# Kernel tuning notes

Measured on AMD Instinct MI355X. Metric: run time of the kernel, lower is better.

Reference implementation:

```python
import jax, jax.numpy as jnp
import numpy as np

EPS_NORM = 1e-12  # torch F.normalize eps
EPS_MM = 1e-08    # min-max denom eps


def setup_inputs() -> dict:
    key = jax.random.key(0)
    k1, k2 = jax.random.split(key)
    global_query = jax.random.normal(k1, (16, 256), dtype=jnp.float32)
    value = jax.random.normal(k2, (16, 256, 128, 128), dtype=jnp.float32)
    return {"global_query": global_query, "value": value}


def reference(global_query, value):
    # L2 normalize (torch.F.normalize: x / max(||x||, eps))
    q = global_query / jnp.maximum(
        jnp.linalg.norm(global_query, axis=-1, keepdims=True), EPS_NORM)
    v = value / jnp.maximum(
        jnp.linalg.norm(value, axis=1, keepdims=True), EPS_NORM)
    B, D, W, H = v.shape
    # score[b, w, h] = sum_d q[b,d] * v[b,d,w,h]  -> [B, W*H]
    score = jnp.einsum('bd,bdwh->bwh', q, v).reshape(B, W * H)
    # min/max computed under no_grad in the original -> stop_gradient
    max_s = jax.lax.stop_gradient(jnp.max(score, axis=1, keepdims=True))
    min_s = jax.lax.stop_gradient(jnp.min(score, axis=1, keepdims=True))
    attn = (score - min_s) / (max_s - min_s + EPS_MM)  # [B, W*H]
    attn = attn.reshape(B, 1, W, H)
    context = attn * v
    return (context, attn)
```

## Files before the change

### kernel.cpp

```cpp
#include <hip/hip_runtime.h>
#include <hip/hip_bf16.h>


#define B_  16
#define D_  256
#define WH_ 16384

__device__ __forceinline__ unsigned int fmap(float f) {
    unsigned int u = __float_as_uint(f);
    return (u & 0x80000000u) ? ~u : (u | 0x80000000u);
}
__device__ __forceinline__ float funmap(unsigned int u) {
    unsigned int b = (u & 0x80000000u) ? (u ^ 0x80000000u) : ~u;
    return __uint_as_float(b);
}

typedef float f32x4_t __attribute__((ext_vector_type(4)));
__device__ __forceinline__ void nt_store4(float* p, float4 v) {
    f32x4_t w = {v.x, v.y, v.z, v.w};
    __builtin_nontemporal_store(w, (f32x4_t*)p);
}

__global__ void init_mm_kernel(unsigned int* __restrict__ mm) {
    int i = threadIdx.x;
    if (i < 2 * B_) mm[i] = (i & 1) ? 0u : 0xFFFFFFFFu;
}

__global__ __launch_bounds__(256) void score_kernel(
    const float* __restrict__ q, const float* __restrict__ value,
    float* __restrict__ score, float* __restrict__ invn,
    unsigned int* __restrict__ mm)
{
    const int b   = blockIdx.y;
    const int tid = threadIdx.x;
    __shared__ float qs[D_];
    __shared__ float red[256];

    float qv = q[b * D_ + tid];
    red[tid] = qv * qv;
    __syncthreads();
    for (int s = 128; s > 0; s >>= 1) {
        if (tid < s) red[tid] += red[tid + s];
        __syncthreads();
    }
    float qnorm2 = red[0];
    __syncthreads();
    qs[tid] = qv * (1.0f / fmaxf(sqrtf(qnorm2), 1e-12f));
    __syncthreads();

    const int wh0 = (blockIdx.x * 256 + tid) * 4;
    const float* vb = value + (size_t)b * D_ * WH_ + wh0;
    float ss0 = 0.f, ss1 = 0.f, ss2 = 0.f, ss3 = 0.f;
    float dt0 = 0.f, dt1 = 0.f, dt2 = 0.f, dt3 = 0.f;
#pragma unroll 4
    for (int d = 0; d < D_; ++d) {
        float4 v4 = *(const float4*)(vb + (size_t)d * WH_);
        float qd = qs[d];
        ss0 += v4.x * v4.x; ss1 += v4.y * v4.y;
        ss2 += v4.z * v4.z; ss3 += v4.w * v4.w;
        dt0 += qd * v4.x;   dt1 += qd * v4.y;
        dt2 += qd * v4.z;   dt3 += qd * v4.w;
    }
    float n0 = 1.0f / fmaxf(sqrtf(ss0), 1e-12f);
    float n1 = 1.0f / fmaxf(sqrtf(ss1), 1e-12f);
    float n2 = 1.0f / fmaxf(sqrtf(ss2), 1e-12f);
    float n3 = 1.0f / fmaxf(sqrtf(ss3), 1e-12f);
    float s0 = dt0 * n0, s1 = dt1 * n1, s2 = dt2 * n2, s3 = dt3 * n3;

    *(float4*)(score + (size_t)b * WH_ + wh0) = make_float4(s0, s1, s2, s3);
    *(float4*)(invn  + (size_t)b * WH_ + wh0) = make_float4(n0, n1, n2, n3);

    float mn = fminf(fminf(s0, s1), fminf(s2, s3));
    float mx = fmaxf(fmaxf(s0, s1), fmaxf(s2, s3));
    red[tid] = mn;
    __syncthreads();
    for (int s = 128; s > 0; s >>= 1) {
        if (tid < s) red[tid] = fminf(red[tid], red[tid + s]);
        __syncthreads();
    }
    float bmn = red[0];
    __syncthreads();
    red[tid] = mx;
    __syncthreads();
    for (int s = 128; s > 0; s >>= 1) {
        if (tid < s) red[tid] = fmaxf(red[tid], red[tid + s]);
        __syncthreads();
    }
    if (tid == 0) {
        atomicMin(&mm[2 * b],     fmap(bmn));
        atomicMax(&mm[2 * b + 1], fmap(red[0]));
    }
}

__global__ __launch_bounds__(256) void ctx_kernel(
    const float* __restrict__ value, const float* __restrict__ score,
    const float* __restrict__ invn, const unsigned int* __restrict__ mm,
    float* __restrict__ out_ctx, float* __restrict__ out_attn)
{
    const int x  = blockIdx.x & (WH_ / 1024 - 1);
    const int dq = blockIdx.x >> 4;
    const int b  = blockIdx.y;
    const int wh0 = (x * 256 + threadIdx.x) * 4;

    const float mn = funmap(mm[2 * b]);
    const float sc = 1.0f / (funmap(mm[2 * b + 1]) - mn + 1e-8f);

    float4 s4 = *(const float4*)(score + (size_t)b * WH_ + wh0);
    float4 n4 = *(const float4*)(invn  + (size_t)b * WH_ + wh0);
    float4 a4;
    a4.x = (s4.x - mn) * sc; a4.y = (s4.y - mn) * sc;
    a4.z = (s4.z - mn) * sc; a4.w = (s4.w - mn) * sc;
    if (dq == 0) nt_store4(out_attn + (size_t)b * WH_ + wh0, a4);

    const float an0 = a4.x * n4.x, an1 = a4.y * n4.y;
    const float an2 = a4.z * n4.z, an3 = a4.w * n4.w;

    const float* vb = value   + (size_t)b * D_ * WH_ + wh0;
    float*       cb = out_ctx + (size_t)b * D_ * WH_ + wh0;
#pragma unroll 4
    for (int d = dq * 64 + 63; d >= dq * 64; --d) {
        float4 v4 = *(const float4*)(vb + (size_t)d * WH_);
        float4 c4;
        c4.x = an0 * v4.x; c4.y = an1 * v4.y;
        c4.z = an2 * v4.z; c4.w = an3 * v4.w;
        nt_store4(cb + (size_t)d * WH_, c4);
    }
}

extern "C" void kernel_launch(void* const* d_in, const int* in_sizes, int n_in,
                              void* d_out, int out_size, void* d_ws, size_t ws_size,
                              hipStream_t stream) {
    const float* q     = (const float*)d_in[0];
    const float* value = (const float*)d_in[1];

    float* out_ctx  = (float*)d_out;
    float* out_attn = out_ctx + (size_t)B_ * D_ * WH_;

    float* score = (float*)d_ws;
    float* invn  = score + (size_t)B_ * WH_;
    unsigned int* mm = (unsigned int*)(invn + (size_t)B_ * WH_);

    hipLaunchKernelGGL(init_mm_kernel, dim3(1), dim3(64), 0, stream, mm);
    hipLaunchKernelGGL(score_kernel, dim3(WH_ / 1024, B_), dim3(256), 0, stream,
                       q, value, score, invn, mm);
    hipLaunchKernelGGL(ctx_kernel, dim3(4 * (WH_ / 1024), B_), dim3(256),
                       0, stream, value, score, invn, mm, out_ctx, out_attn);
}
```

Measured before the change: 136.1 us.

## Split score kernel channel reduction across four waves per block with LDS combine

The score kernel now uses 1024 threads per block, with each group of 256 threads reducing a quarter of the 256 channels. Partial sums of squares and dot products go to shared memory and are combined by the first group. The goal is more memory-level parallelism in a grid of only 256 blocks, which underfills the GPU. The ctx kernel now walks the channel quarters in reverse so it starts on the data the score kernel read last, which is likely still in cache, and both loops unroll more. The cost is extra LDS traffic, more barriers, and idle threads during the reductions.

```diff
diff --git a/kernel.cpp b/kernel.cpp
--- a/kernel.cpp
+++ b/kernel.cpp
@@ -26,64 +26,84 @@
     if (i < 2 * B_) mm[i] = (i & 1) ? 0u : 0xFFFFFFFFu;
 }
 
-__global__ __launch_bounds__(256) void score_kernel(
+__global__ __launch_bounds__(1024) void score_kernel(
     const float* __restrict__ q, const float* __restrict__ value,
     float* __restrict__ score, float* __restrict__ invn,
     unsigned int* __restrict__ mm)
 {
     const int b   = blockIdx.y;
     const int tid = threadIdx.x;
+    const int whl = tid & 255;
+    const int dq  = tid >> 8;
+
     __shared__ float qs[D_];
     __shared__ float red[256];
+    __shared__ float part[3 * 256 * 9];
 
-    float qv = q[b * D_ + tid];
-    red[tid] = qv * qv;
+    float qv = 0.f;
+    if (dq == 0) { qv = q[b * D_ + whl]; red[whl] = qv * qv; }
     __syncthreads();
     for (int s = 128; s > 0; s >>= 1) {
-        if (tid < s) red[tid] += red[tid + s];
+        if (dq == 0 && whl < s) red[whl] += red[whl + s];
         __syncthreads();
     }
-    float qnorm2 = red[0];
-    __syncthreads();
-    qs[tid] = qv * (1.0f / fmaxf(sqrtf(qnorm2), 1e-12f));
+    if (dq == 0) qs[whl] = qv * (1.0f / fmaxf(sqrtf(red[0]), 1e-12f));
     __syncthreads();
 
-    const int wh0 = (blockIdx.x * 256 + tid) * 4;
-    const float* vb = value + (size_t)b * D_ * WH_ + wh0;
+    const int wh0 = (blockIdx.x * 256 + whl) * 4;
+    const float* vb = value + ((size_t)b * D_ + (size_t)dq * 64) * WH_ + wh0;
     float ss0 = 0.f, ss1 = 0.f, ss2 = 0.f, ss3 = 0.f;
     float dt0 = 0.f, dt1 = 0.f, dt2 = 0.f, dt3 = 0.f;
-#pragma unroll 4
-    for (int d = 0; d < D_; ++d) {
+#pragma unroll 16
+    for (int d = 0; d < 64; ++d) {
         float4 v4 = *(const float4*)(vb + (size_t)d * WH_);
-        float qd = qs[d];
+        float qd = qs[dq * 64 + d];
         ss0 += v4.x * v4.x; ss1 += v4.y * v4.y;
         ss2 += v4.z * v4.z; ss3 += v4.w * v4.w;
         dt0 += qd * v4.x;   dt1 += qd * v4.y;
         dt2 += qd * v4.z;   dt3 += qd * v4.w;
     }
-    float n0 = 1.0f / fmaxf(sqrtf(ss0), 1e-12f);
-    float n1 = 1.0f / fmaxf(sqrtf(ss1), 1e-12f);
-    float n2 = 1.0f / fmaxf(sqrtf(ss2), 1e-12f);
-    float n3 = 1.0f / fmaxf(sqrtf(ss3), 1e-12f);
-    float s0 = dt0 * n0, s1 = dt1 * n1, s2 = dt2 * n2, s3 = dt3 * n3;
 
-    *(float4*)(score + (size_t)b * WH_ + wh0) = make_float4(s0, s1, s2, s3);
-    *(float4*)(invn  + (size_t)b * WH_ + wh0) = make_float4(n0, n1, n2, n3);
+    if (dq > 0) {
+        float* p = &part[((dq - 1) * 256 + whl) * 9];
+        p[0] = ss0; p[1] = ss1; p[2] = ss2; p[3] = ss3;
+        p[4] = dt0; p[5] = dt1; p[6] = dt2; p[7] = dt3;
+    }
+    __syncthreads();
 
-    float mn = fminf(fminf(s0, s1), fminf(s2, s3));
-    float mx = fmaxf(fmaxf(s0, s1), fmaxf(s2, s3));
-    red[tid] = mn;
+    float mn = 0.f, mx = 0.f;
+    if (dq == 0) {
+#pragma unroll
+        for (int c = 0; c < 3; ++c) {
+            const float* p = &part[(c * 256 + whl) * 9];
+            ss0 += p[0]; ss1 += p[1]; ss2 += p[2]; ss3 += p[3];
+            dt0 += p[4]; dt1 += p[5]; dt2 += p[6]; dt3 += p[7];
+        }
+        float n0 = 1.0f / fmaxf(sqrtf(ss0), 1e-12f);
+        float n1 = 1.0f / fmaxf(sqrtf(ss1), 1e-12f);
+        float n2 = 1.0f / fmaxf(sqrtf(ss2), 1e-12f);
+        float n3 = 1.0f / fmaxf(sqrtf(ss3), 1e-12f);
+        float s0 = dt0 * n0, s1 = dt1 * n1, s2 = dt2 * n2, s3 = dt3 * n3;
+
+        *(float4*)(score + (size_t)b * WH_ + wh0) = make_float4(s0, s1, s2, s3);
+        *(float4*)(invn  + (size_t)b * WH_ + wh0) = make_float4(n0, n1, n2, n3);
+
+        mn = fminf(fminf(s0, s1), fminf(s2, s3));
+        mx = fmaxf(fmaxf(s0, s1), fmaxf(s2, s3));
+    }
+
+    if (dq == 0) red[whl] = mn;
     __syncthreads();
     for (int s = 128; s > 0; s >>= 1) {
-        if (tid < s) red[tid] = fminf(red[tid], red[tid + s]);
+        if (dq == 0 && whl < s) red[whl] = fminf(red[whl], red[whl + s]);
         __syncthreads();
     }
     float bmn = red[0];
     __syncthreads();
-    red[tid] = mx;
+    if (dq == 0) red[whl] = mx;
     __syncthreads();
     for (int s = 128; s > 0; s >>= 1) {
-        if (tid < s) red[tid] = fmaxf(red[tid], red[tid + s]);
+        if (dq == 0 && whl < s) red[whl] = fmaxf(red[whl], red[whl + s]);
         __syncthreads();
     }
     if (tid == 0) {
@@ -98,7 +118,7 @@
     float* __restrict__ out_ctx, float* __restrict__ out_attn)
 {
     const int x  = blockIdx.x & (WH_ / 1024 - 1);
-    const int dq = blockIdx.x >> 4;
+    const int dq = 3 - (blockIdx.x >> 4);
     const int b  = blockIdx.y;
     const int wh0 = (x * 256 + threadIdx.x) * 4;
 
@@ -117,7 +137,7 @@
 
     const float* vb = value   + (size_t)b * D_ * WH_ + wh0;
     float*       cb = out_ctx + (size_t)b * D_ * WH_ + wh0;
-#pragma unroll 4
+#pragma unroll 16
     for (int d = dq * 64 + 63; d >= dq * 64; --d) {
         float4 v4 = *(const float4*)(vb + (size_t)d * WH_);
         float4 c4;
@@ -141,7 +161,7 @@
     unsigned int* mm = (unsigned int*)(invn + (size_t)B_ * WH_);
 
     hipLaunchKernelGGL(init_mm_kernel, dim3(1), dim3(64), 0, stream, mm);
-    hipLaunchKernelGGL(score_kernel, dim3(WH_ / 1024, B_), dim3(256), 0, stream,
+    hipLaunchKernelGGL(score_kernel, dim3(WH_ / 1024, B_), dim3(1024), 0, stream,
                        q, value, score, invn, mm);
     hipLaunchKernelGGL(ctx_kernel, dim3(4 * (WH_ / 1024), B_), dim3(256),
                        0, stream, value, score, invn, mm, out_ctx, out_attn);
```

Result: slower. 148.8 us (+9.3%).

## Fuse score and context into persistent kernel with per-batch grid barrier

Applied to the files above, without the earlier changes.

The separate score and context kernels are replaced by one persistent kernel of 256 blocks. Each block owns a 64-column slice and loops over batches, splitting the D reduction across 16 thread groups and reducing through shared memory. Per-batch arrival counters act as a grid barrier for the global min/max, and the context pass for batch b-1 runs right after the score pass for batch b, so the second read of value can likely hit cache. This removes the score and inverse-norm workspace round-trip. The cost is one resident block per CU (low occupancy), serialising spin-waits, 256-byte strided row accesses, and reliance on all blocks being co-resident to avoid deadlock.

```diff
diff --git a/kernel.cpp b/kernel.cpp
--- a/kernel.cpp
+++ b/kernel.cpp
@@ -2,9 +2,11 @@
 #include <hip/hip_bf16.h>
 
 
-#define B_  16
-#define D_  256
-#define WH_ 16384
+#define B_   16
+#define D_   256
+#define WH_  16384
+#define NBLK 256
+#define WPB  64
 
 __device__ __forceinline__ unsigned int fmap(float f) {
     unsigned int u = __float_as_uint(f);
@@ -21,109 +23,175 @@
     __builtin_nontemporal_store(w, (f32x4_t*)p);
 }
 
-__global__ void init_mm_kernel(unsigned int* __restrict__ mm) {
+__global__ void init_kernel(unsigned int* __restrict__ mm,
+                            unsigned int* __restrict__ cnt) {
     int i = threadIdx.x;
     if (i < 2 * B_) mm[i] = (i & 1) ? 0u : 0xFFFFFFFFu;
-}
-
-__global__ __launch_bounds__(256) void score_kernel(
+    if (i < B_) cnt[i] = 0u;
+}
+
+__global__ __launch_bounds__(256) void fused_kernel(
     const float* __restrict__ q, const float* __restrict__ value,
-    float* __restrict__ score, float* __restrict__ invn,
-    unsigned int* __restrict__ mm)
+    unsigned int* __restrict__ mm, unsigned int* __restrict__ cnt,
+    float* __restrict__ out_ctx, float* __restrict__ out_attn)
 {
-    const int b   = blockIdx.y;
-    const int tid = threadIdx.x;
+    const int tid  = threadIdx.x;
+    const int col  = tid & 15;
+    const int dgrp = tid >> 4;
+    const int whb  = blockIdx.x * WPB;
+
     __shared__ float qs[D_];
     __shared__ float red[256];
-
-    float qv = q[b * D_ + tid];
-    red[tid] = qv * qv;
-    __syncthreads();
-    for (int s = 128; s > 0; s >>= 1) {
-        if (tid < s) red[tid] += red[tid + s];
-        __syncthreads();
+    __shared__ float part[16][16][9];
+    __shared__ float scL[2][WPB], ivL[2][WPB];
+    __shared__ float bmn_s, bsc_s;
+
+    const size_t slice_off = (size_t)whb + (size_t)col * 4;
+
+    for (int b = 0; b < B_; ++b) {
+        const int pb = b & 1;
+        float qv = q[b * D_ + tid];
+        red[tid] = qv * qv;
+        __syncthreads();
+        for (int s = 128; s > 0; s >>= 1) {
+            if (tid < s) red[tid] += red[tid + s];
+            __syncthreads();
+        }
+        float qinv = 1.0f / fmaxf(sqrtf(red[0]), 1e-12f);
+        __syncthreads();
+        qs[tid] = qv * qinv;
+        __syncthreads();
+
+        const float* vb = value + ((size_t)b * D_ + dgrp * 16) * WH_ + slice_off;
+        float ss0 = 0.f, ss1 = 0.f, ss2 = 0.f, ss3 = 0.f;
+        float dt0 = 0.f, dt1 = 0.f, dt2 = 0.f, dt3 = 0.f;
+#pragma unroll
+        for (int k = 0; k < 16; ++k) {
+            float4 v4 = *(const float4*)(vb + (size_t)k * WH_);
+            float qd = qs[dgrp * 16 + k];
+            ss0 += v4.x * v4.x; ss1 += v4.y * v4.y;
+            ss2 += v4.z * v4.z; ss3 += v4.w * v4.w;
+            dt0 += qd * v4.x;   dt1 += qd * v4.y;
+            dt2 += qd * v4.z;   dt3 += qd * v4.w;
+        }
+        float* p = &part[dgrp][col][0];
+        p[0] = ss0; p[1] = ss1; p[2] = ss2; p[3] = ss3;
+        p[4] = dt0; p[5] = dt1; p[6] = dt2; p[7] = dt3;
+        __syncthreads();
+        for (int s = 8; s >= 1; s >>= 1) {
+            if (dgrp < s) {
+#pragma unroll
+                for (int j = 0; j < 8; ++j)
+                    part[dgrp][col][j] += part[dgrp + s][col][j];
+            }
+            __syncthreads();
+        }
+        if (tid < 16) {
+            const float* t8 = &part[0][tid][0];
+            float n0 = 1.0f / fmaxf(sqrtf(t8[0]), 1e-12f);
+            float n1 = 1.0f / fmaxf(sqrtf(t8[1]), 1e-12f);
+            float n2 = 1.0f / fmaxf(sqrtf(t8[2]), 1e-12f);
+            float n3 = 1.0f / fmaxf(sqrtf(t8[3]), 1e-12f);
+            float s0 = t8[4] * n0, s1 = t8[5] * n1;
+            float s2 = t8[6] * n2, s3 = t8[7] * n3;
+            scL[pb][tid * 4 + 0] = s0; ivL[pb][tid * 4 + 0] = n0;
+            scL[pb][tid * 4 + 1] = s1; ivL[pb][tid * 4 + 1] = n1;
+            scL[pb][tid * 4 + 2] = s2; ivL[pb][tid * 4 + 2] = n2;
+            scL[pb][tid * 4 + 3] = s3; ivL[pb][tid * 4 + 3] = n3;
+            red[tid]      = fminf(fminf(s0, s1), fminf(s2, s3));
+            red[16 + tid] = fmaxf(fmaxf(s0, s1), fmaxf(s2, s3));
+        }
+        __syncthreads();
+        if (tid == 0) {
+            float mn = red[0], mx = red[16];
+            for (int i = 1; i < 16; ++i) {
+                mn = fminf(mn, red[i]); mx = fmaxf(mx, red[16 + i]);
+            }
+            atomicMin(&mm[2 * b],     fmap(mn));
+            atomicMax(&mm[2 * b + 1], fmap(mx));
+            __hip_atomic_fetch_add(&cnt[b], 1u, __ATOMIC_ACQ_REL,
+                                   __HIP_MEMORY_SCOPE_AGENT);
+        }
+
+        if (b > 0) {
+            const int c  = b - 1;
+            const int pc = c & 1;
+            if (tid == 0) {
+                while (__hip_atomic_load(&cnt[c], __ATOMIC_ACQUIRE,
+                                         __HIP_MEMORY_SCOPE_AGENT) < NBLK)
+                    __builtin_amdgcn_s_sleep(2);
+                unsigned um = __hip_atomic_load(&mm[2 * c], __ATOMIC_ACQUIRE,
+                                                __HIP_MEMORY_SCOPE_AGENT);
+                unsigned ux = __hip_atomic_load(&mm[2 * c + 1], __ATOMIC_ACQUIRE,
+                                                __HIP_MEMORY_SCOPE_AGENT);
+                float mnv = funmap(um);
+                bmn_s = mnv;
+                bsc_s = 1.0f / (funmap(ux) - mnv + 1e-8f);
+            }
+            __syncthreads();
+            float mnv = bmn_s, scv = bsc_s;
+            float a0 = (scL[pc][col * 4 + 0] - mnv) * scv;
+            float a1 = (scL[pc][col * 4 + 1] - mnv) * scv;
+            float a2 = (scL[pc][col * 4 + 2] - mnv) * scv;
+            float a3 = (scL[pc][col * 4 + 3] - mnv) * scv;
+            if (tid < 16)
+                nt_store4(out_attn + (size_t)c * WH_ + whb + tid * 4,
+                          make_float4(a0, a1, a2, a3));
+            float an0 = a0 * ivL[pc][col * 4 + 0];
+            float an1 = a1 * ivL[pc][col * 4 + 1];
+            float an2 = a2 * ivL[pc][col * 4 + 2];
+            float an3 = a3 * ivL[pc][col * 4 + 3];
+            const float* vc = value   + ((size_t)c * D_ + dgrp * 16) * WH_ + slice_off;
+            float*       oc = out_ctx + ((size_t)c * D_ + dgrp * 16) * WH_ + slice_off;
+#pragma unroll
+            for (int k = 0; k < 16; ++k) {
+                float4 v4 = *(const float4*)(vc + (size_t)k * WH_);
+                float4 c4;
+                c4.x = an0 * v4.x; c4.y = an1 * v4.y;
+                c4.z = an2 * v4.z; c4.w = an3 * v4.w;
+                nt_store4(oc + (size_t)k * WH_, c4);
+            }
+            __syncthreads();
+        }
     }
-    float qnorm2 = red[0];
-    __syncthreads();
-    qs[tid] = qv * (1.0f / fmaxf(sqrtf(qnorm2), 1e-12f));
-    __syncthreads();
-
-    const int wh0 = (blockIdx.x * 256 + tid) * 4;
-    const float* vb = value + (size_t)b * D_ * WH_ + wh0;
-    float ss0 = 0.f, ss1 = 0.f, ss2 = 0.f, ss3 = 0.f;
-    float dt0 = 0.f, dt1 = 0.f, dt2 = 0.f, dt3 = 0.f;
-#pragma unroll 4
-    for (int d = 0; d < D_; ++d) {
-        float4 v4 = *(const float4*)(vb + (size_t)d * WH_);
-        float qd = qs[d];
-        ss0 += v4.x * v4.x; ss1 += v4.y * v4.y;
-        ss2 += v4.z * v4.z; ss3 += v4.w * v4.w;
-        dt0 += qd * v4.x;   dt1 += qd * v4.y;
-        dt2 += qd * v4.z;   dt3 += qd * v4.w;
-    }
-    float n0 = 1.0f / fmaxf(sqrtf(ss0), 1e-12f);
-    float n1 = 1.0f / fmaxf(sqrtf(ss1), 1e-12f);
-    float n2 = 1.0f / fmaxf(sqrtf(ss2), 1e-12f);
-    float n3 = 1.0f / fmaxf(sqrtf(ss3), 1e-12f);
-    float s0 = dt0 * n0, s1 = dt1 * n1, s2 = dt2 * n2, s3 = dt3 * n3;
-
-    *(float4*)(score + (size_t)b * WH_ + wh0) = make_float4(s0, s1, s2, s3);
-    *(float4*)(invn  + (size_t)b * WH_ + wh0) = make_float4(n0, n1, n2, n3);
-
-    float mn = fminf(fminf(s0, s1), fminf(s2, s3));
-    float mx = fmaxf(fmaxf(s0, s1), fmaxf(s2, s3));
-    red[tid] = mn;
-    __syncthreads();
-    for (int s = 128; s > 0; s >>= 1) {
-        if (tid < s) red[tid] = fminf(red[tid], red[tid + s]);
-        __syncthreads();
-    }
-    float bmn = red[0];
-    __syncthreads();
-    red[tid] = mx;
-    __syncthreads();
-    for (int s = 128; s > 0; s >>= 1) {
-        if (tid < s) red[tid] = fmaxf(red[tid], red[tid + s]);
-        __syncthreads();
-    }
-    if (tid == 0) {
-        atomicMin(&mm[2 * b],     fmap(bmn));
-        atomicMax(&mm[2 * b + 1], fmap(red[0]));
-    }
-}
-
-__global__ __launch_bounds__(256) void ctx_kernel(
-    const float* __restrict__ value, const float* __restrict__ score,
-    const float* __restrict__ invn, const unsigned int* __restrict__ mm,
-    float* __restrict__ out_ctx, float* __restrict__ out_attn)
-{
-    const int x  = blockIdx.x & (WH_ / 1024 - 1);
-    const int dq = blockIdx.x >> 4;
-    const int b  = blockIdx.y;
-    const int wh0 = (x * 256 + threadIdx.x) * 4;
-
-    const float mn = funmap(mm[2 * b]);
-    const float sc = 1.0f / (funmap(mm[2 * b + 1]) - mn + 1e-8f);
-
-    float4 s4 = *(const float4*)(score + (size_t)b * WH_ + wh0);
-    float4 n4 = *(const float4*)(invn  + (size_t)b * WH_ + wh0);
-    float4 a4;
-    a4.x = (s4.x - mn) * sc; a4.y = (s4.y - mn) * sc;
-    a4.z = (s4.z - mn) * sc; a4.w = (s4.w - mn) * sc;
-    if (dq == 0) nt_store4(out_attn + (size_t)b * WH_ + wh0, a4);
-
-    const float an0 = a4.x * n4.x, an1 = a4.y * n4.y;
-    const float an2 = a4.z * n4.z, an3 = a4.w * n4.w;
-
-    const float* vb = value   + (size_t)b * D_ * WH_ + wh0;
-    float*       cb = out_ctx + (size_t)b * D_ * WH_ + wh0;
-#pragma unroll 4
-    for (int d = dq * 64 + 63; d >= dq * 64; --d) {
-        float4 v4 = *(const float4*)(vb + (size_t)d * WH_);
-        float4 c4;
-        c4.x = an0 * v4.x; c4.y = an1 * v4.y;
-        c4.z = an2 * v4.z; c4.w = an3 * v4.w;
-        nt_store4(cb + (size_t)d * WH_, c4);
+
+    {
+        const int c = B_ - 1, pc = c & 1;
+        if (tid == 0) {
+            while (__hip_atomic_load(&cnt[c], __ATOMIC_ACQUIRE,
+                                     __HIP_MEMORY_SCOPE_AGENT) < NBLK)
+                __builtin_amdgcn_s_sleep(2);
+            unsigned um = __hip_atomic_load(&mm[2 * c], __ATOMIC_ACQUIRE,
+                                            __HIP_MEMORY_SCOPE_AGENT);
+            unsigned ux = __hip_atomic_load(&mm[2 * c + 1], __ATOMIC_ACQUIRE,
+                                            __HIP_MEMORY_SCOPE_AGENT);
+            float mnv = funmap(um);
+            bmn_s = mnv;
+            bsc_s = 1.0f / (funmap(ux) - mnv + 1e-8f);
+        }
+        __syncthreads();
+        float mnv = bmn_s, scv = bsc_s;
+        float a0 = (scL[pc][col * 4 + 0] - mnv) * scv;
+        float a1 = (scL[pc][col * 4 + 1] - mnv) * scv;
+        float a2 = (scL[pc][col * 4 + 2] - mnv) * scv;
+        float a3 = (scL[pc][col * 4 + 3] - mnv) * scv;
+        if (tid < 16)
+            nt_store4(out_attn + (size_t)c * WH_ + whb + tid * 4,
+                      make_float4(a0, a1, a2, a3));
+        float an0 = a0 * ivL[pc][col * 4 + 0];
+        float an1 = a1 * ivL[pc][col * 4 + 1];
+        float an2 = a2 * ivL[pc][col * 4 + 2];
+        float an3 = a3 * ivL[pc][col * 4 + 3];
+        const float* vc = value   + ((size_t)c * D_ + dgrp * 16) * WH_ + slice_off;
+        float*       oc = out_ctx + ((size_t)c * D_ + dgrp * 16) * WH_ + slice_off;
+#pragma unroll
+        for (int k = 0; k < 16; ++k) {
+            float4 v4 = *(const float4*)(vc + (size_t)k * WH_);
+            float4 c4;
+            c4.x = an0 * v4.x; c4.y = an1 * v4.y;
+            c4.z = an2 * v4.z; c4.w = an3 * v4.w;
+            nt_store4(oc + (size_t)k * WH_, c4);
+        }
     }
 }
 
@@ -136,13 +204,10 @@
     float* out_ctx  = (float*)d_out;
     float* out_attn = out_ctx + (size_t)B_ * D_ * WH_;
 
-    float* score = (float*)d_ws;
-    float* invn  = score + (size_t)B_ * WH_;
-    unsigned int* mm = (unsigned int*)(invn + (size_t)B_ * WH_);
-
-    hipLaunchKernelGGL(init_mm_kernel, dim3(1), dim3(64), 0, stream, mm);
-    hipLaunchKernelGGL(score_kernel, dim3(WH_ / 1024, B_), dim3(256), 0, stream,
-                       q, value, score, invn, mm);
-    hipLaunchKernelGGL(ctx_kernel, dim3(4 * (WH_ / 1024), B_), dim3(256),
-                       0, stream, value, score, invn, mm, out_ctx, out_attn);
-}
+    unsigned int* mm  = (unsigned int*)d_ws;
+    unsigned int* cnt = mm + 2 * B_;
+
+    hipLaunchKernelGGL(init_kernel, dim3(1), dim3(64), 0, stream, mm, cnt);
+    hipLaunchKernelGGL(fused_kernel, dim3(NBLK), dim3(256), 0, stream,
+                       q, value, mm, cnt, out_ctx, out_attn);
+}
```

Result: slower. 330.5 us (+142.8%).
